# Performance work log

Measured on AMD Instinct MI355X. Metric: run time of the kernel, lower is better.

## Reference

```python
import jax, jax.numpy as jnp
import numpy as np

B, A, L, D, H = 8, 16, 80, 128, 6  # scenes, agents/scene, lanes/scene, feat dim, heads
LN_EPS = 1e-5


def _build_edges():
    hi_l, wi_l = [], []
    n_agt = B * A
    for b in range(B):
        ids = np.concatenate([np.arange(b * A, (b + 1) * A),
                              n_agt + np.arange(b * L, (b + 1) * L)])
        n = len(ids)
        hi_l.append(np.repeat(ids, n))  # 'd -> (d n)'
        wi_l.append(np.tile(ids, n))    # 'd -> (n d)'
    return (jnp.asarray(np.concatenate(hi_l), dtype=jnp.int32),
            jnp.asarray(np.concatenate(wi_l), dtype=jnp.int32))


def setup_inputs() -> dict:
    key = jax.random.key(0)
    ks = jax.random.split(key, 10)
    w = 0.05  # small init so exp(att) is well-behaved
    hi, wi = _build_edges()
    return {
        "agents": jax.random.normal(ks[0], (B * A, D), jnp.float32),
        "lanes": jax.random.normal(ks[1], (B * L, D), jnp.float32),
        "Wq": w * jax.random.normal(ks[2], (D, H * D), jnp.float32),
        "Wk": w * jax.random.normal(ks[3], (D, H * D), jnp.float32),
        "Wv": w * jax.random.normal(ks[4], (D, H * D), jnp.float32),
        "Wout1": w * jax.random.normal(ks[5], (H * D, D), jnp.float32),
        "Wout2": w * jax.random.normal(ks[6], (D, D), jnp.float32),
        "W1": w * jax.random.normal(ks[7], (D, D), jnp.float32),
        "ln_g": jnp.ones((D,), jnp.float32),
        "ln_b": jnp.zeros((D,), jnp.float32),
        "W2": w * jax.random.normal(ks[8], (D, D), jnp.float32),
        "hi": hi,
        "wi": wi,
    }


def _layernorm(x, g, b):
    mu = x.mean(-1, keepdims=True)
    var = ((x - mu) ** 2).mean(-1, keepdims=True)
    return (x - mu) * jax.lax.rsqrt(var + LN_EPS) * g + b


def reference(agents, lanes, Wq, Wk, Wv, Wout1, Wout2, W1, ln_g, ln_b, W2, hi, wi):
    nodes = jnp.concatenate([agents, lanes], axis=0)  # [N, D]
    N = nodes.shape[0]
    n_agt = agents.shape[0]
    scale = D ** -0.5

    src = nodes[hi]  # [E, D] (query side)
    dst = nodes[wi]  # [E, D] (key/value side)
    q = (src @ Wq).reshape(-1, H, D)
    k = (dst @ Wk).reshape(-1, H, D)
    v = jax.nn.relu(dst @ Wv).reshape(-1, H, D)

    att = jnp.einsum('ehd,ehd->eh', q, k) * scale          # [E, H]
    att = jnp.exp(att - att.max())                          # global-max-shifted exp (as in source)
    denom = jax.ops.segment_sum(att, hi, num_segments=N)    # [N, H]
    att = att / denom[hi]
    out = jax.ops.segment_sum(att[..., None] * v, hi, num_segments=N)  # [N, H, D]
    out = out.reshape(N, H * D)

    out = jax.nn.relu(out @ Wout1) @ Wout2                  # to_out
    h = _layernorm(nodes @ W1 + out, ln_g, ln_b)
    h = jax.nn.relu(h)
    h = h @ W2
    h = jax.nn.relu(h + nodes)                              # residual to pre-attention nodes
    return h[:n_agt]
```

## Files before the change

kernel.cpp:

```cpp
#include <hip/hip_runtime.h>
#include <math.h>

#define LN_EPS 1e-5f


__global__ __launch_bounds__(256) void k_prep(
    const float* __restrict__ Wq, const float* __restrict__ Wk,
    const float* __restrict__ agents, const float* __restrict__ W1,
    float* __restrict__ M, float* __restrict__ base)
{
    __shared__ float As[128][68];
    __shared__ float Bs[128][68];

    const int tid = threadIdx.x;
    const int bid = blockIdx.x;

    float* dst;
    if (bid < 24) {
        const int h = bid >> 2, quad = bid & 3;
        const int i0 = (quad >> 1) * 64, j0 = (quad & 1) * 64;
        const int c4 = tid & 15, kr = tid >> 4;
        #pragma unroll
        for (int ii = 0; ii < 8; ++ii) {
            const int k = kr + 16 * ii;
            *(float4*)&As[k][c4 * 4] =
                *(const float4*)(Wq + (size_t)k * 768 + h * 128 + i0 + c4 * 4);
            *(float4*)&Bs[k][c4 * 4] =
                *(const float4*)(Wk + (size_t)k * 768 + h * 128 + j0 + c4 * 4);
        }
        dst = M + (size_t)h * 16384 + (size_t)i0 * 128 + j0;
    } else {
        const int quad = bid - 24;
        const int i0 = (quad >> 1) * 64, j0 = (quad & 1) * 64;
        const int row = tid >> 2, kq = tid & 3;
        #pragma unroll
        for (int j = 0; j < 8; ++j) {
            const int k0 = kq * 4 + j * 16;
            const float4 a = *(const float4*)(agents + (size_t)(i0 + row) * 128 + k0);
            As[k0 + 0][row] = a.x; As[k0 + 1][row] = a.y;
            As[k0 + 2][row] = a.z; As[k0 + 3][row] = a.w;
        }
        const int c4 = tid & 15, kr = tid >> 4;
        #pragma unroll
        for (int ii = 0; ii < 8; ++ii) {
            const int k = kr + 16 * ii;
            *(float4*)&Bs[k][c4 * 4] =
                *(const float4*)(W1 + (size_t)k * 128 + j0 + c4 * 4);
        }
        dst = base + (size_t)i0 * 128 + j0;
    }
    __syncthreads();

    const int tx = tid & 15, ty = tid >> 4;
    float acc[4][4] = {};
    #pragma unroll 8
    for (int k = 0; k < 128; ++k) {
        const float4 a = *(const float4*)&As[k][ty * 4];
        const float4 b = *(const float4*)&Bs[k][tx * 4];
        const float av[4] = {a.x, a.y, a.z, a.w};
        #pragma unroll
        for (int i = 0; i < 4; ++i) {
            acc[i][0] += av[i] * b.x; acc[i][1] += av[i] * b.y;
            acc[i][2] += av[i] * b.z; acc[i][3] += av[i] * b.w;
        }
    }
    #pragma unroll
    for (int i = 0; i < 4; ++i)
        *(float4*)(dst + (size_t)(ty * 4 + i) * 128 + tx * 4) =
            make_float4(acc[i][0], acc[i][1], acc[i][2], acc[i][3]);
}

__global__ __launch_bounds__(512) void k_attn_f(
    const float* __restrict__ agents, const float* __restrict__ lanes,
    const float* __restrict__ Wv, const float* __restrict__ M,
    float* __restrict__ AO)
{
    __shared__ float Ns[96][132];
    __shared__ float Vh[96][68];
    __shared__ float Tt[16][132];
    __shared__ float Sm[16][100];

    const int tid = threadIdx.x;
    const int b = blockIdx.x;
    const int s = b / 12, r12 = b % 12;
    const int h = r12 >> 1, half = r12 & 1;

    for (int idx = tid; idx < 96 * 32; idx += 512) {
        const int n = idx >> 5, c4 = idx & 31;
        const float* src = (n < 16) ? (agents + (size_t)(s * 16 + n) * 128)
                                    : (lanes + (size_t)(s * 80 + n - 16) * 128);
        *(float4*)&Ns[n][c4 * 4] = *(const float4*)(src + c4 * 4);
    }
    __syncthreads();

    {
        const int c4 = tid & 15, rg = tid >> 4;
        const float* wp = Wv + h * 128 + half * 64 + c4 * 4;
        float4 a0 = make_float4(0,0,0,0), a1 = a0, a2 = a0;
        #pragma unroll 8
        for (int k = 0; k < 128; ++k) {
            const float4 w = *(const float4*)(wp + (size_t)k * 768);
            const float n0 = Ns[rg][k], n1 = Ns[rg + 32][k], n2 = Ns[rg + 64][k];
            a0.x += n0 * w.x; a0.y += n0 * w.y; a0.z += n0 * w.z; a0.w += n0 * w.w;
            a1.x += n1 * w.x; a1.y += n1 * w.y; a1.z += n1 * w.z; a1.w += n1 * w.w;
            a2.x += n2 * w.x; a2.y += n2 * w.y; a2.z += n2 * w.z; a2.w += n2 * w.w;
        }
        a0.x = fmaxf(a0.x, 0.f); a0.y = fmaxf(a0.y, 0.f);
        a0.z = fmaxf(a0.z, 0.f); a0.w = fmaxf(a0.w, 0.f);
        a1.x = fmaxf(a1.x, 0.f); a1.y = fmaxf(a1.y, 0.f);
        a1.z = fmaxf(a1.z, 0.f); a1.w = fmaxf(a1.w, 0.f);
        a2.x = fmaxf(a2.x, 0.f); a2.y = fmaxf(a2.y, 0.f);
        a2.z = fmaxf(a2.z, 0.f); a2.w = fmaxf(a2.w, 0.f);
        *(float4*)&Vh[rg][c4 * 4]      = a0;
        *(float4*)&Vh[rg + 32][c4 * 4] = a1;
        *(float4*)&Vh[rg + 64][c4 * 4] = a2;
    }

    {
        const int c4 = tid & 31, r = tid >> 5;
        const float* mp = M + (size_t)h * 16384 + c4 * 4;
        float4 acc = make_float4(0,0,0,0);
        #pragma unroll 8
        for (int k = 0; k < 128; ++k) {
            const float4 m4 = *(const float4*)(mp + (size_t)k * 128);
            const float a = Ns[r][k];
            acc.x += a * m4.x; acc.y += a * m4.y;
            acc.z += a * m4.z; acc.w += a * m4.w;
        }
        *(float4*)&Tt[r][c4 * 4] = acc;
    }
    __syncthreads();

    {
        const int i = tid >> 5, jc = tid & 31;
        float s0 = 0, s1 = 0, s2 = 0;
        #pragma unroll 4
        for (int kk = 0; kk < 32; ++kk) {
            const float4 t4 = *(const float4*)&Tt[i][kk * 4];
            const float4 a  = *(const float4*)&Ns[jc][kk * 4];
            const float4 bb = *(const float4*)&Ns[jc + 32][kk * 4];
            const float4 c  = *(const float4*)&Ns[jc + 64][kk * 4];
            s0 += t4.x*a.x  + t4.y*a.y  + t4.z*a.z  + t4.w*a.w;
            s1 += t4.x*bb.x + t4.y*bb.y + t4.z*bb.z + t4.w*bb.w;
            s2 += t4.x*c.x  + t4.y*c.y  + t4.z*c.z  + t4.w*c.w;
        }
        const float scale = 0.088388347648318447f;
        s0 *= scale; s1 *= scale; s2 *= scale;
        float m = fmaxf(fmaxf(s0, s1), s2);
        #pragma unroll
        for (int o = 16; o >= 1; o >>= 1) m = fmaxf(m, __shfl_xor(m, o, 32));
        const float e0 = __expf(s0 - m), e1 = __expf(s1 - m), e2 = __expf(s2 - m);
        float sum = e0 + e1 + e2;
        #pragma unroll
        for (int o = 16; o >= 1; o >>= 1) sum += __shfl_xor(sum, o, 32);
        const float inv = 1.0f / sum;
        Sm[i][jc]      = e0 * inv;
        Sm[i][jc + 32] = e1 * inv;
        Sm[i][jc + 64] = e2 * inv;
    }

    {
        const int i = tid >> 5, d2 = tid & 31;
        float o0 = 0, o1 = 0;
        #pragma unroll 4
        for (int j = 0; j < 96; ++j) {
            const float p = Sm[i][j];
            const float2 v = *(const float2*)&Vh[j][2 * d2];
            o0 += p * v.x; o1 += p * v.y;
        }
        float* dst = AO + (size_t)(s * 16 + i) * 768 + h * 128 + half * 64 + 2 * d2;
        *(float2*)dst = make_float2(o0, o1);
    }
}

__global__ __launch_bounds__(256) void k_f1(
    const float* __restrict__ AO, const float* __restrict__ Wout1,
    float* __restrict__ y1p)
{
    __shared__ float As[128][68];
    __shared__ float Bs[128][68];

    const int tid = threadIdx.x;
    const int b = blockIdx.x;
    const int s6 = b >> 2, quad = b & 3;
    const int m0 = (quad >> 1) * 64, n0 = (quad & 1) * 64;

    {
        const int row = tid >> 2, kq = tid & 3;
        #pragma unroll
        for (int j = 0; j < 8; ++j) {
            const int k0 = kq * 4 + j * 16;
            const float4 a =
                *(const float4*)(AO + (size_t)(m0 + row) * 768 + s6 * 128 + k0);
            As[k0 + 0][row] = a.x; As[k0 + 1][row] = a.y;
            As[k0 + 2][row] = a.z; As[k0 + 3][row] = a.w;
        }
    }
    {
        const int c4 = tid & 15, kr = tid >> 4;
        #pragma unroll
        for (int ii = 0; ii < 8; ++ii) {
            const int k = kr + 16 * ii;
            *(float4*)&Bs[k][c4 * 4] =
                *(const float4*)(Wout1 + (size_t)(s6 * 128 + k) * 128 + n0 + c4 * 4);
        }
    }
    __syncthreads();

    const int tx = tid & 15, ty = tid >> 4;
    float acc[4][4] = {};
    #pragma unroll 8
    for (int k = 0; k < 128; ++k) {
        const float4 a = *(const float4*)&As[k][ty * 4];
        const float4 bv = *(const float4*)&Bs[k][tx * 4];
        const float av[4] = {a.x, a.y, a.z, a.w};
        #pragma unroll
        for (int i = 0; i < 4; ++i) {
            acc[i][0] += av[i] * bv.x; acc[i][1] += av[i] * bv.y;
            acc[i][2] += av[i] * bv.z; acc[i][3] += av[i] * bv.w;
        }
    }
    float* dst = y1p + (size_t)s6 * 16384 + (size_t)m0 * 128 + n0;
    #pragma unroll
    for (int i = 0; i < 4; ++i)
        *(float4*)(dst + (size_t)(ty * 4 + i) * 128 + tx * 4) =
            make_float4(acc[i][0], acc[i][1], acc[i][2], acc[i][3]);
}

__global__ __launch_bounds__(512) void k_f2(
    const float* __restrict__ y1p, const float* __restrict__ base,
    const float* __restrict__ agents, const float* __restrict__ Wout2,
    const float* __restrict__ ln_g, const float* __restrict__ ln_b,
    const float* __restrict__ W2, float* __restrict__ out)
{
    const int a = blockIdx.x;
    const int tid = threadIdx.x;
    __shared__ float y1s[128];
    __shared__ float nr[128];
    __shared__ float br[128];
    __shared__ float hb[128];
    __shared__ float ps[512];
    __shared__ float red[4];

    if (tid < 32) {
        float4 acc = make_float4(0,0,0,0);
        #pragma unroll
        for (int s6 = 0; s6 < 6; ++s6) {
            const float4 v =
                *(const float4*)(y1p + (size_t)s6 * 16384 + (size_t)a * 128 + tid * 4);
            acc.x += v.x; acc.y += v.y; acc.z += v.z; acc.w += v.w;
        }
        y1s[tid * 4 + 0] = fmaxf(acc.x, 0.f); y1s[tid * 4 + 1] = fmaxf(acc.y, 0.f);
        y1s[tid * 4 + 2] = fmaxf(acc.z, 0.f); y1s[tid * 4 + 3] = fmaxf(acc.w, 0.f);
    } else if (tid < 64) {
        const int t = tid - 32;
        *(float4*)&nr[t * 4] = *(const float4*)(agents + (size_t)a * 128 + t * 4);
    } else if (tid < 96) {
        const int t = tid - 64;
        *(float4*)&br[t * 4] = *(const float4*)(base + (size_t)a * 128 + t * 4);
    }
    __syncthreads();

    const int d = tid & 127, g = tid >> 7;
    {
        const int k0 = g * 32;
        float p = 0.f;
        #pragma unroll 8
        for (int k = 0; k < 32; ++k)
            p += y1s[k0 + k] * Wout2[(size_t)(k0 + k) * 128 + d];
        ps[tid] = p;
    }
    __syncthreads();

    float tval = 0.f;
    if (tid < 128) tval = ps[d] + ps[128 + d] + ps[256 + d] + ps[384 + d] + br[d];
    float s1 = tval, s2 = tval * tval;
    #pragma unroll
    for (int o = 32; o >= 1; o >>= 1) { s1 += __shfl_xor(s1, o); s2 += __shfl_xor(s2, o); }
    if (tid < 128 && (tid & 63) == 0) {
        red[(tid >> 6) * 2] = s1; red[(tid >> 6) * 2 + 1] = s2;
    }
    __syncthreads();
    if (tid < 128) {
        const float S1 = red[0] + red[2], S2 = red[1] + red[3];
        const float mu  = S1 * (1.0f / 128.0f);
        const float var = S2 * (1.0f / 128.0f) - mu * mu;
        const float rin = rsqrtf(var + LN_EPS);
        hb[tid] = fmaxf((tval - mu) * rin * ln_g[tid] + ln_b[tid], 0.0f);
    }
    __syncthreads();

    {
        const int k0 = g * 32;
        float p = 0.f;
        #pragma unroll 8
        for (int k = 0; k < 32; ++k)
            p += hb[k0 + k] * W2[(size_t)(k0 + k) * 128 + d];
        ps[tid] = p;
    }
    __syncthreads();
    if (tid < 128)
        out[(size_t)a * 128 + d] =
            fmaxf(ps[d] + ps[128 + d] + ps[256 + d] + ps[384 + d] + nr[d], 0.0f);
}

extern "C" void kernel_launch(void* const* d_in, const int* in_sizes, int n_in,
                              void* d_out, int out_size, void* d_ws, size_t ws_size,
                              hipStream_t stream)
{
    const float* agents = (const float*)d_in[0];
    const float* lanes  = (const float*)d_in[1];
    const float* Wq     = (const float*)d_in[2];
    const float* Wk     = (const float*)d_in[3];
    const float* Wv     = (const float*)d_in[4];
    const float* Wout1  = (const float*)d_in[5];
    const float* Wout2  = (const float*)d_in[6];
    const float* W1     = (const float*)d_in[7];
    const float* ln_g   = (const float*)d_in[8];
    const float* ln_b   = (const float*)d_in[9];
    const float* W2     = (const float*)d_in[10];

    float* ws = (float*)d_ws;
    float* M    = ws;
    float* base = M + 6 * 16384;
    float* AO   = base + 16384;
    float* y1p  = AO + 128 * 768;
    float* outp = (float*)d_out;

    k_prep  <<<28, 256, 0, stream>>>(Wq, Wk, agents, W1, M, base);
    k_attn_f<<<96, 512, 0, stream>>>(agents, lanes, Wv, M, AO);
    k_f1    <<<24, 256, 0, stream>>>(AO, Wout1, y1p);
    k_f2    <<<128, 512, 0, stream>>>(y1p, base, agents, Wout2, ln_g, ln_b, W2, outp);
}
```

Baseline: 117.4 us.

## Precompute V and Q projections in a wide GEMM, compute Q·Wk^T in attention

The prep kernel no longer builds per-head Wq·Wk^T matrices. It now computes relu(nodes·Wv) for all nodes and agents·Wq with a 172-block tiled GEMM. The attention kernel loads the precomputed V and Q slices, and forms Q·Wk_h^T in 32-row chunks of Wk staged through shared memory, instead of running a per-block V projection and an M multiply. The Wout1 split-K GEMM is split more finely (48 blocks over 64-wide K slices), and the final kernel sums 12 partials instead of 6. This spreads the work over more blocks for parallelism, at the cost of writing V and Q through global memory and adding extra syncs in the attention kernel.

```diff
diff --git a/kernel.cpp b/kernel.cpp
--- a/kernel.cpp
+++ b/kernel.cpp
@@ -4,10 +4,11 @@
 #define LN_EPS 1e-5f
 
 
-__global__ __launch_bounds__(256) void k_prep(
-    const float* __restrict__ Wq, const float* __restrict__ Wk,
-    const float* __restrict__ agents, const float* __restrict__ W1,
-    float* __restrict__ M, float* __restrict__ base)
+__global__ __launch_bounds__(256) void k_qv(
+    const float* __restrict__ agents, const float* __restrict__ lanes,
+    const float* __restrict__ Wv, const float* __restrict__ Wq,
+    const float* __restrict__ W1, float* __restrict__ V,
+    float* __restrict__ Qb, float* __restrict__ base)
 {
     __shared__ float As[128][68];
     __shared__ float Bs[128][68];
@@ -15,39 +16,45 @@
     const int tid = threadIdx.x;
     const int bid = blockIdx.x;
 
-    float* dst;
-    if (bid < 24) {
-        const int h = bid >> 2, quad = bid & 3;
-        const int i0 = (quad >> 1) * 64, j0 = (quad & 1) * 64;
-        const int c4 = tid & 15, kr = tid >> 4;
-        #pragma unroll
-        for (int ii = 0; ii < 8; ++ii) {
-            const int k = kr + 16 * ii;
-            *(float4*)&As[k][c4 * 4] =
-                *(const float4*)(Wq + (size_t)k * 768 + h * 128 + i0 + c4 * 4);
-            *(float4*)&Bs[k][c4 * 4] =
-                *(const float4*)(Wk + (size_t)k * 768 + h * 128 + j0 + c4 * 4);
-        }
-        dst = M + (size_t)h * 16384 + (size_t)i0 * 128 + j0;
+    const float* W;
+    float* Out;
+    int r0, wc0, wstride, dstride;
+    bool dorelu = false;
+    if (bid < 144) {
+        const int br = bid % 12, bc = bid / 12;
+        r0 = br * 64; W = Wv; wc0 = bc * 64; wstride = 768;
+        Out = V; dstride = 768; dorelu = true;
+    } else if (bid < 168) {
+        const int idx = bid - 144;
+        r0 = (idx & 1) * 64; W = Wq; wc0 = (idx >> 1) * 64; wstride = 768;
+        Out = Qb; dstride = 768;
     } else {
-        const int quad = bid - 24;
-        const int i0 = (quad >> 1) * 64, j0 = (quad & 1) * 64;
-        const int row = tid >> 2, kq = tid & 3;
+        const int idx = bid - 168;
+        r0 = (idx & 1) * 64; W = W1; wc0 = (idx >> 1) * 64; wstride = 128;
+        Out = base; dstride = 128;
+    }
+
+    {
+        const int row = tid >> 2, kv = tid & 3;
+        const int gr = r0 + row;
+        const float* src = (gr < 128) ? (agents + (size_t)gr * 128)
+                                      : (lanes + (size_t)(gr - 128) * 128);
         #pragma unroll
         for (int j = 0; j < 8; ++j) {
-            const int k0 = kq * 4 + j * 16;
-            const float4 a = *(const float4*)(agents + (size_t)(i0 + row) * 128 + k0);
+            const int k0 = kv * 4 + j * 16;
+            const float4 a = *(const float4*)(src + k0);
             As[k0 + 0][row] = a.x; As[k0 + 1][row] = a.y;
             As[k0 + 2][row] = a.z; As[k0 + 3][row] = a.w;
         }
-        const int c4 = tid & 15, kr = tid >> 4;
-        #pragma unroll
-        for (int ii = 0; ii < 8; ++ii) {
-            const int k = kr + 16 * ii;
+    }
+    {
+        const int kr = tid >> 4, c4 = tid & 15;
+        #pragma unroll
+        for (int i = 0; i < 8; ++i) {
+            const int k = kr + 16 * i;
             *(float4*)&Bs[k][c4 * 4] =
-                *(const float4*)(W1 + (size_t)k * 128 + j0 + c4 * 4);
-        }
-        dst = base + (size_t)i0 * 128 + j0;
+                *(const float4*)(W + (size_t)k * wstride + wc0 + c4 * 4);
+        }
     }
     __syncthreads();
 
@@ -65,74 +72,85 @@
         }
     }
     #pragma unroll
-    for (int i = 0; i < 4; ++i)
-        *(float4*)(dst + (size_t)(ty * 4 + i) * 128 + tx * 4) =
-            make_float4(acc[i][0], acc[i][1], acc[i][2], acc[i][3]);
-}
-
-__global__ __launch_bounds__(512) void k_attn_f(
+    for (int i = 0; i < 4; ++i) {
+        float4 v = make_float4(acc[i][0], acc[i][1], acc[i][2], acc[i][3]);
+        if (dorelu) {
+            v.x = fmaxf(v.x, 0.f); v.y = fmaxf(v.y, 0.f);
+            v.z = fmaxf(v.z, 0.f); v.w = fmaxf(v.w, 0.f);
+        }
+        *(float4*)(Out + (size_t)(r0 + ty * 4 + i) * dstride + wc0 + tx * 4) = v;
+    }
+}
+
+__global__ __launch_bounds__(512) void k_attn2(
     const float* __restrict__ agents, const float* __restrict__ lanes,
-    const float* __restrict__ Wv, const float* __restrict__ M,
-    float* __restrict__ AO)
+    const float* __restrict__ Wk, const float* __restrict__ V,
+    const float* __restrict__ Qb, float* __restrict__ AO)
 {
     __shared__ float Ns[96][132];
     __shared__ float Vh[96][68];
+    __shared__ float Qs[16][132];
     __shared__ float Tt[16][132];
     __shared__ float Sm[16][100];
+    __shared__ float Wc[32][132];
 
     const int tid = threadIdx.x;
     const int b = blockIdx.x;
     const int s = b / 12, r12 = b % 12;
     const int h = r12 >> 1, half = r12 & 1;
 
-    for (int idx = tid; idx < 96 * 32; idx += 512) {
+    #pragma unroll
+    for (int ii = 0; ii < 6; ++ii) {
+        const int idx = tid + ii * 512;
         const int n = idx >> 5, c4 = idx & 31;
         const float* src = (n < 16) ? (agents + (size_t)(s * 16 + n) * 128)
                                     : (lanes + (size_t)(s * 80 + n - 16) * 128);
         *(float4*)&Ns[n][c4 * 4] = *(const float4*)(src + c4 * 4);
     }
-    __syncthreads();
-
-    {
-        const int c4 = tid & 15, rg = tid >> 4;
-        const float* wp = Wv + h * 128 + half * 64 + c4 * 4;
-        float4 a0 = make_float4(0,0,0,0), a1 = a0, a2 = a0;
-        #pragma unroll 8
-        for (int k = 0; k < 128; ++k) {
-            const float4 w = *(const float4*)(wp + (size_t)k * 768);
-            const float n0 = Ns[rg][k], n1 = Ns[rg + 32][k], n2 = Ns[rg + 64][k];
-            a0.x += n0 * w.x; a0.y += n0 * w.y; a0.z += n0 * w.z; a0.w += n0 * w.w;
-            a1.x += n1 * w.x; a1.y += n1 * w.y; a1.z += n1 * w.z; a1.w += n1 * w.w;
-            a2.x += n2 * w.x; a2.y += n2 * w.y; a2.z += n2 * w.z; a2.w += n2 * w.w;
-        }
-        a0.x = fmaxf(a0.x, 0.f); a0.y = fmaxf(a0.y, 0.f);
-        a0.z = fmaxf(a0.z, 0.f); a0.w = fmaxf(a0.w, 0.f);
-        a1.x = fmaxf(a1.x, 0.f); a1.y = fmaxf(a1.y, 0.f);
-        a1.z = fmaxf(a1.z, 0.f); a1.w = fmaxf(a1.w, 0.f);
-        a2.x = fmaxf(a2.x, 0.f); a2.y = fmaxf(a2.y, 0.f);
-        a2.z = fmaxf(a2.z, 0.f); a2.w = fmaxf(a2.w, 0.f);
-        *(float4*)&Vh[rg][c4 * 4]      = a0;
-        *(float4*)&Vh[rg + 32][c4 * 4] = a1;
-        *(float4*)&Vh[rg + 64][c4 * 4] = a2;
-    }
-
-    {
-        const int c4 = tid & 31, r = tid >> 5;
-        const float* mp = M + (size_t)h * 16384 + c4 * 4;
-        float4 acc = make_float4(0,0,0,0);
-        #pragma unroll 8
-        for (int k = 0; k < 128; ++k) {
-            const float4 m4 = *(const float4*)(mp + (size_t)k * 128);
-            const float a = Ns[r][k];
-            acc.x += a * m4.x; acc.y += a * m4.y;
-            acc.z += a * m4.z; acc.w += a * m4.w;
-        }
-        *(float4*)&Tt[r][c4 * 4] = acc;
-    }
-    __syncthreads();
-
-    {
-        const int i = tid >> 5, jc = tid & 31;
+    #pragma unroll
+    for (int ii = 0; ii < 3; ++ii) {
+        const int idx = tid + ii * 512;
+        const int n = idx >> 4, c4 = idx & 15;
+        const int g = (n < 16) ? (s * 16 + n) : (128 + s * 80 + (n - 16));
+        *(float4*)&Vh[n][c4 * 4] =
+            *(const float4*)(V + (size_t)g * 768 + h * 128 + half * 64 + c4 * 4);
+    }
+    {
+        const int r = tid >> 5, c4 = tid & 31;
+        *(float4*)&Qs[r][c4 * 4] =
+            *(const float4*)(Qb + (size_t)(s * 16 + r) * 768 + h * 128 + c4 * 4);
+    }
+    __syncthreads();
+
+    const int r = tid >> 5, kc = tid & 31;
+    for (int ck = 0; ck < 4; ++ck) {
+        {
+            const int i0 = tid * 2;
+            #pragma unroll
+            for (int ii = 0; ii < 2; ++ii) {
+                const int idx = i0 + ii;
+                const int row = idx >> 5, c4 = idx & 31;
+                *(float4*)&Wc[row][c4 * 4] =
+                    *(const float4*)(Wk + (size_t)(ck * 32 + row) * 768 +
+                                     h * 128 + c4 * 4);
+            }
+        }
+        __syncthreads();
+        {
+            float acc = 0.f;
+            #pragma unroll 8
+            for (int c4 = 0; c4 < 32; ++c4) {
+                const float4 q = *(const float4*)&Qs[r][c4 * 4];
+                const float4 w = *(const float4*)&Wc[kc][c4 * 4];
+                acc += q.x * w.x + q.y * w.y + q.z * w.z + q.w * w.w;
+            }
+            Tt[r][ck * 32 + kc] = acc;
+        }
+        __syncthreads();
+    }
+
+    {
+        const int i = r, jc = kc;
         float s0 = 0, s1 = 0, s2 = 0;
         #pragma unroll 4
         for (int kk = 0; kk < 32; ++kk) {
@@ -160,49 +178,49 @@
     }
 
     {
-        const int i = tid >> 5, d2 = tid & 31;
+        const int i = r, d = kc;
         float o0 = 0, o1 = 0;
         #pragma unroll 4
         for (int j = 0; j < 96; ++j) {
             const float p = Sm[i][j];
-            const float2 v = *(const float2*)&Vh[j][2 * d2];
+            const float2 v = *(const float2*)&Vh[j][2 * d];
             o0 += p * v.x; o1 += p * v.y;
         }
-        float* dst = AO + (size_t)(s * 16 + i) * 768 + h * 128 + half * 64 + 2 * d2;
+        float* dst = AO + (size_t)(s * 16 + i) * 768 + h * 128 + half * 64 + 2 * d;
         *(float2*)dst = make_float2(o0, o1);
     }
 }
 
-__global__ __launch_bounds__(256) void k_f1(
+__global__ __launch_bounds__(256) void k_f1w(
     const float* __restrict__ AO, const float* __restrict__ Wout1,
     float* __restrict__ y1p)
 {
-    __shared__ float As[128][68];
-    __shared__ float Bs[128][68];
+    __shared__ float As[64][68];
+    __shared__ float Bs[64][68];
 
     const int tid = threadIdx.x;
     const int b = blockIdx.x;
-    const int s6 = b >> 2, quad = b & 3;
+    const int ks = b >> 2, quad = b & 3;
     const int m0 = (quad >> 1) * 64, n0 = (quad & 1) * 64;
 
     {
         const int row = tid >> 2, kq = tid & 3;
         #pragma unroll
-        for (int j = 0; j < 8; ++j) {
+        for (int j = 0; j < 4; ++j) {
             const int k0 = kq * 4 + j * 16;
             const float4 a =
-                *(const float4*)(AO + (size_t)(m0 + row) * 768 + s6 * 128 + k0);
+                *(const float4*)(AO + (size_t)(m0 + row) * 768 + ks * 64 + k0);
             As[k0 + 0][row] = a.x; As[k0 + 1][row] = a.y;
             As[k0 + 2][row] = a.z; As[k0 + 3][row] = a.w;
         }
     }
     {
-        const int c4 = tid & 15, kr = tid >> 4;
-        #pragma unroll
-        for (int ii = 0; ii < 8; ++ii) {
-            const int k = kr + 16 * ii;
+        const int kr = tid >> 4, c4 = tid & 15;
+        #pragma unroll
+        for (int i = 0; i < 4; ++i) {
+            const int k = kr + 16 * i;
             *(float4*)&Bs[k][c4 * 4] =
-                *(const float4*)(Wout1 + (size_t)(s6 * 128 + k) * 128 + n0 + c4 * 4);
+                *(const float4*)(Wout1 + (size_t)(ks * 64 + k) * 128 + n0 + c4 * 4);
         }
     }
     __syncthreads();
@@ -210,7 +228,7 @@
     const int tx = tid & 15, ty = tid >> 4;
     float acc[4][4] = {};
     #pragma unroll 8
-    for (int k = 0; k < 128; ++k) {
+    for (int k = 0; k < 64; ++k) {
         const float4 a = *(const float4*)&As[k][ty * 4];
         const float4 bv = *(const float4*)&Bs[k][tx * 4];
         const float av[4] = {a.x, a.y, a.z, a.w};
@@ -220,7 +238,7 @@
             acc[i][2] += av[i] * bv.z; acc[i][3] += av[i] * bv.w;
         }
     }
-    float* dst = y1p + (size_t)s6 * 16384 + (size_t)m0 * 128 + n0;
+    float* dst = y1p + (size_t)ks * 16384 + (size_t)m0 * 128 + n0;
     #pragma unroll
     for (int i = 0; i < 4; ++i)
         *(float4*)(dst + (size_t)(ty * 4 + i) * 128 + tx * 4) =
@@ -245,9 +263,9 @@
     if (tid < 32) {
         float4 acc = make_float4(0,0,0,0);
         #pragma unroll
-        for (int s6 = 0; s6 < 6; ++s6) {
+        for (int ks = 0; ks < 12; ++ks) {
             const float4 v =
-                *(const float4*)(y1p + (size_t)s6 * 16384 + (size_t)a * 128 + tid * 4);
+                *(const float4*)(y1p + (size_t)ks * 16384 + (size_t)a * 128 + tid * 4);
             acc.x += v.x; acc.y += v.y; acc.z += v.z; acc.w += v.w;
         }
         y1s[tid * 4 + 0] = fmaxf(acc.x, 0.f); y1s[tid * 4 + 1] = fmaxf(acc.y, 0.f);
@@ -321,14 +339,15 @@
     const float* W2     = (const float*)d_in[10];
 
     float* ws = (float*)d_ws;
-    float* M    = ws;
-    float* base = M + 6 * 16384;
+    float* V    = ws;
+    float* Qb   = V + 768 * 768;
+    float* base = Qb + 128 * 768;
     float* AO   = base + 16384;
     float* y1p  = AO + 128 * 768;
     float* outp = (float*)d_out;
 
-    k_prep  <<<28, 256, 0, stream>>>(Wq, Wk, agents, W1, M, base);
-    k_attn_f<<<96, 512, 0, stream>>>(agents, lanes, Wv, M, AO);
-    k_f1    <<<24, 256, 0, stream>>>(AO, Wout1, y1p);
-    k_f2    <<<128, 512, 0, stream>>>(y1p, base, agents, Wout2, ln_g, ln_b, W2, outp);
-}
+    k_qv   <<<172, 256, 0, stream>>>(agents, lanes, Wv, Wq, W1, V, Qb, base);
+    k_attn2<<<96, 512, 0, stream>>>(agents, lanes, Wk, V, Qb, AO);
+    k_f1w  <<<48, 256, 0, stream>>>(AO, Wout1, y1p);
+    k_f2   <<<128, 512, 0, stream>>>(y1p, base, agents, Wout2, ln_g, ln_b, W2, outp);
+}
```

After: 107.9 us. 1.09x faster.

## Fuse pipeline into two kernels, computing Q/K projections inside attention

Applied to the files above, without the earlier changes.

Removes the precomputed Wq·Wk^T product kernel. The attention kernel now computes the query projection per agent, then the query-times-Wk^T product, staging weight chunks in shared memory. The Wout1 GEMM and the nodes·W1 term move into the per-agent tail kernel, so the partial-sum workspace buffers and two launches go away. This cuts launch count and intermediate global traffic, but each tail block now reads all of Wout1 and attention blocks redo some projection work.

```diff
diff --git a/kernel.cpp b/kernel.cpp
--- a/kernel.cpp
+++ b/kernel.cpp
@@ -4,135 +4,116 @@
 #define LN_EPS 1e-5f
 
 
-__global__ __launch_bounds__(256) void k_prep(
+__global__ __launch_bounds__(512) void k_attn_all(
+    const float* __restrict__ agents, const float* __restrict__ lanes,
     const float* __restrict__ Wq, const float* __restrict__ Wk,
-    const float* __restrict__ agents, const float* __restrict__ W1,
-    float* __restrict__ M, float* __restrict__ base)
-{
-    __shared__ float As[128][68];
-    __shared__ float Bs[128][68];
-
-    const int tid = threadIdx.x;
-    const int bid = blockIdx.x;
-
-    float* dst;
-    if (bid < 24) {
-        const int h = bid >> 2, quad = bid & 3;
-        const int i0 = (quad >> 1) * 64, j0 = (quad & 1) * 64;
-        const int c4 = tid & 15, kr = tid >> 4;
-        #pragma unroll
-        for (int ii = 0; ii < 8; ++ii) {
-            const int k = kr + 16 * ii;
-            *(float4*)&As[k][c4 * 4] =
-                *(const float4*)(Wq + (size_t)k * 768 + h * 128 + i0 + c4 * 4);
-            *(float4*)&Bs[k][c4 * 4] =
-                *(const float4*)(Wk + (size_t)k * 768 + h * 128 + j0 + c4 * 4);
-        }
-        dst = M + (size_t)h * 16384 + (size_t)i0 * 128 + j0;
-    } else {
-        const int quad = bid - 24;
-        const int i0 = (quad >> 1) * 64, j0 = (quad & 1) * 64;
-        const int row = tid >> 2, kq = tid & 3;
-        #pragma unroll
-        for (int j = 0; j < 8; ++j) {
-            const int k0 = kq * 4 + j * 16;
-            const float4 a = *(const float4*)(agents + (size_t)(i0 + row) * 128 + k0);
-            As[k0 + 0][row] = a.x; As[k0 + 1][row] = a.y;
-            As[k0 + 2][row] = a.z; As[k0 + 3][row] = a.w;
-        }
-        const int c4 = tid & 15, kr = tid >> 4;
-        #pragma unroll
-        for (int ii = 0; ii < 8; ++ii) {
-            const int k = kr + 16 * ii;
-            *(float4*)&Bs[k][c4 * 4] =
-                *(const float4*)(W1 + (size_t)k * 128 + j0 + c4 * 4);
-        }
-        dst = base + (size_t)i0 * 128 + j0;
-    }
-    __syncthreads();
-
-    const int tx = tid & 15, ty = tid >> 4;
-    float acc[4][4] = {};
-    #pragma unroll 8
-    for (int k = 0; k < 128; ++k) {
-        const float4 a = *(const float4*)&As[k][ty * 4];
-        const float4 b = *(const float4*)&Bs[k][tx * 4];
-        const float av[4] = {a.x, a.y, a.z, a.w};
-        #pragma unroll
-        for (int i = 0; i < 4; ++i) {
-            acc[i][0] += av[i] * b.x; acc[i][1] += av[i] * b.y;
-            acc[i][2] += av[i] * b.z; acc[i][3] += av[i] * b.w;
-        }
-    }
-    #pragma unroll
-    for (int i = 0; i < 4; ++i)
-        *(float4*)(dst + (size_t)(ty * 4 + i) * 128 + tx * 4) =
-            make_float4(acc[i][0], acc[i][1], acc[i][2], acc[i][3]);
-}
-
-__global__ __launch_bounds__(512) void k_attn_f(
-    const float* __restrict__ agents, const float* __restrict__ lanes,
-    const float* __restrict__ Wv, const float* __restrict__ M,
-    float* __restrict__ AO)
+    const float* __restrict__ Wv, float* __restrict__ AO)
 {
     __shared__ float Ns[96][132];
     __shared__ float Vh[96][68];
+    __shared__ float Qs[16][132];
     __shared__ float Tt[16][132];
     __shared__ float Sm[16][100];
+    __shared__ float Wc[64][132];
 
     const int tid = threadIdx.x;
     const int b = blockIdx.x;
     const int s = b / 12, r12 = b % 12;
     const int h = r12 >> 1, half = r12 & 1;
 
-    for (int idx = tid; idx < 96 * 32; idx += 512) {
+    #pragma unroll
+    for (int ii = 0; ii < 6; ++ii) {
+        const int idx = tid + ii * 512;
         const int n = idx >> 5, c4 = idx & 31;
         const float* src = (n < 16) ? (agents + (size_t)(s * 16 + n) * 128)
                                     : (lanes + (size_t)(s * 80 + n - 16) * 128);
         *(float4*)&Ns[n][c4 * 4] = *(const float4*)(src + c4 * 4);
     }
-    __syncthreads();
-
-    {
-        const int c4 = tid & 15, rg = tid >> 4;
-        const float* wp = Wv + h * 128 + half * 64 + c4 * 4;
-        float4 a0 = make_float4(0,0,0,0), a1 = a0, a2 = a0;
-        #pragma unroll 8
-        for (int k = 0; k < 128; ++k) {
-            const float4 w = *(const float4*)(wp + (size_t)k * 768);
-            const float n0 = Ns[rg][k], n1 = Ns[rg + 32][k], n2 = Ns[rg + 64][k];
-            a0.x += n0 * w.x; a0.y += n0 * w.y; a0.z += n0 * w.z; a0.w += n0 * w.w;
-            a1.x += n1 * w.x; a1.y += n1 * w.y; a1.z += n1 * w.z; a1.w += n1 * w.w;
-            a2.x += n2 * w.x; a2.y += n2 * w.y; a2.z += n2 * w.z; a2.w += n2 * w.w;
-        }
-        a0.x = fmaxf(a0.x, 0.f); a0.y = fmaxf(a0.y, 0.f);
-        a0.z = fmaxf(a0.z, 0.f); a0.w = fmaxf(a0.w, 0.f);
-        a1.x = fmaxf(a1.x, 0.f); a1.y = fmaxf(a1.y, 0.f);
-        a1.z = fmaxf(a1.z, 0.f); a1.w = fmaxf(a1.w, 0.f);
-        a2.x = fmaxf(a2.x, 0.f); a2.y = fmaxf(a2.y, 0.f);
-        a2.z = fmaxf(a2.z, 0.f); a2.w = fmaxf(a2.w, 0.f);
-        *(float4*)&Vh[rg][c4 * 4]      = a0;
-        *(float4*)&Vh[rg + 32][c4 * 4] = a1;
-        *(float4*)&Vh[rg + 64][c4 * 4] = a2;
-    }
-
-    {
-        const int c4 = tid & 31, r = tid >> 5;
-        const float* mp = M + (size_t)h * 16384 + c4 * 4;
-        float4 acc = make_float4(0,0,0,0);
-        #pragma unroll 8
-        for (int k = 0; k < 128; ++k) {
-            const float4 m4 = *(const float4*)(mp + (size_t)k * 128);
-            const float a = Ns[r][k];
-            acc.x += a * m4.x; acc.y += a * m4.y;
-            acc.z += a * m4.z; acc.w += a * m4.w;
-        }
-        *(float4*)&Tt[r][c4 * 4] = acc;
-    }
-    __syncthreads();
-
-    {
-        const int i = tid >> 5, jc = tid & 31;
+
+    const int r = tid >> 5, jc = tid & 31;
+
+    float q0 = 0, q1 = 0, q2 = 0, q3 = 0;
+    for (int ck = 0; ck < 2; ++ck) {
+        __syncthreads();
+        #pragma unroll
+        for (int ii = 0; ii < 4; ++ii) {
+            const int idx = tid + ii * 512;
+            const int row = idx >> 5, c4 = idx & 31;
+            *(float4*)&Wc[row][c4 * 4] =
+                *(const float4*)(Wq + (size_t)(ck * 64 + row) * 768 + h * 128 + c4 * 4);
+        }
+        __syncthreads();
+        #pragma unroll 4
+        for (int kk = 0; kk < 64; ++kk) {
+            const float a = Ns[r][ck * 64 + kk];
+            q0 += a * Wc[kk][jc];
+            q1 += a * Wc[kk][jc + 32];
+            q2 += a * Wc[kk][jc + 64];
+            q3 += a * Wc[kk][jc + 96];
+        }
+    }
+    Qs[r][jc] = q0; Qs[r][jc + 32] = q1; Qs[r][jc + 64] = q2; Qs[r][jc + 96] = q3;
+
+    const int rg = tid >> 4, cv = tid & 15;
+    float4 va0 = make_float4(0,0,0,0), va1 = va0, va2 = va0;
+    for (int ck = 0; ck < 2; ++ck) {
+        __syncthreads();
+        #pragma unroll
+        for (int ii = 0; ii < 2; ++ii) {
+            const int idx = tid + ii * 512;
+            const int row = idx >> 4, cc = idx & 15;
+            *(float4*)&Wc[row][cc * 4] =
+                *(const float4*)(Wv + (size_t)(ck * 64 + row) * 768 +
+                                 h * 128 + half * 64 + cc * 4);
+        }
+        __syncthreads();
+        #pragma unroll 4
+        for (int kk = 0; kk < 64; ++kk) {
+            const float4 w = *(const float4*)&Wc[kk][cv * 4];
+            const float n0 = Ns[rg][ck * 64 + kk];
+            const float n1 = Ns[rg + 32][ck * 64 + kk];
+            const float n2 = Ns[rg + 64][ck * 64 + kk];
+            va0.x += n0 * w.x; va0.y += n0 * w.y; va0.z += n0 * w.z; va0.w += n0 * w.w;
+            va1.x += n1 * w.x; va1.y += n1 * w.y; va1.z += n1 * w.z; va1.w += n1 * w.w;
+            va2.x += n2 * w.x; va2.y += n2 * w.y; va2.z += n2 * w.z; va2.w += n2 * w.w;
+        }
+    }
+    va0.x = fmaxf(va0.x, 0.f); va0.y = fmaxf(va0.y, 0.f);
+    va0.z = fmaxf(va0.z, 0.f); va0.w = fmaxf(va0.w, 0.f);
+    va1.x = fmaxf(va1.x, 0.f); va1.y = fmaxf(va1.y, 0.f);
+    va1.z = fmaxf(va1.z, 0.f); va1.w = fmaxf(va1.w, 0.f);
+    va2.x = fmaxf(va2.x, 0.f); va2.y = fmaxf(va2.y, 0.f);
+    va2.z = fmaxf(va2.z, 0.f); va2.w = fmaxf(va2.w, 0.f);
+    *(float4*)&Vh[rg][cv * 4]      = va0;
+    *(float4*)&Vh[rg + 32][cv * 4] = va1;
+    *(float4*)&Vh[rg + 64][cv * 4] = va2;
+
+    for (int ck = 0; ck < 2; ++ck) {
+        __syncthreads();
+        #pragma unroll
+        for (int ii = 0; ii < 4; ++ii) {
+            const int idx = tid + ii * 512;
+            const int row = idx >> 5, c4 = idx & 31;
+            *(float4*)&Wc[row][c4 * 4] =
+                *(const float4*)(Wk + (size_t)(ck * 64 + row) * 768 + h * 128 + c4 * 4);
+        }
+        __syncthreads();
+        float a1 = 0, a2 = 0;
+        #pragma unroll 4
+        for (int c4i = 0; c4i < 32; ++c4i) {
+            const float4 q  = *(const float4*)&Qs[r][c4i * 4];
+            const float4 w1 = *(const float4*)&Wc[jc][c4i * 4];
+            const float4 w2 = *(const float4*)&Wc[jc + 32][c4i * 4];
+            a1 += q.x * w1.x + q.y * w1.y + q.z * w1.z + q.w * w1.w;
+            a2 += q.x * w2.x + q.y * w2.y + q.z * w2.z + q.w * w2.w;
+        }
+        Tt[r][ck * 64 + jc]      = a1;
+        Tt[r][ck * 64 + 32 + jc] = a2;
+    }
+    __syncthreads();
+
+    {
+        const int i = r;
         float s0 = 0, s1 = 0, s2 = 0;
         #pragma unroll 4
         for (int kk = 0; kk < 32; ++kk) {
@@ -160,120 +141,71 @@
     }
 
     {
-        const int i = tid >> 5, d2 = tid & 31;
+        const int i = r, d = jc;
         float o0 = 0, o1 = 0;
         #pragma unroll 4
         for (int j = 0; j < 96; ++j) {
             const float p = Sm[i][j];
-            const float2 v = *(const float2*)&Vh[j][2 * d2];
+            const float2 v = *(const float2*)&Vh[j][2 * d];
             o0 += p * v.x; o1 += p * v.y;
         }
-        float* dst = AO + (size_t)(s * 16 + i) * 768 + h * 128 + half * 64 + 2 * d2;
+        float* dst = AO + (size_t)(s * 16 + i) * 768 + h * 128 + half * 64 + 2 * d;
         *(float2*)dst = make_float2(o0, o1);
     }
 }
 
-__global__ __launch_bounds__(256) void k_f1(
-    const float* __restrict__ AO, const float* __restrict__ Wout1,
-    float* __restrict__ y1p)
-{
-    __shared__ float As[128][68];
-    __shared__ float Bs[128][68];
-
-    const int tid = threadIdx.x;
-    const int b = blockIdx.x;
-    const int s6 = b >> 2, quad = b & 3;
-    const int m0 = (quad >> 1) * 64, n0 = (quad & 1) * 64;
-
-    {
-        const int row = tid >> 2, kq = tid & 3;
-        #pragma unroll
-        for (int j = 0; j < 8; ++j) {
-            const int k0 = kq * 4 + j * 16;
-            const float4 a =
-                *(const float4*)(AO + (size_t)(m0 + row) * 768 + s6 * 128 + k0);
-            As[k0 + 0][row] = a.x; As[k0 + 1][row] = a.y;
-            As[k0 + 2][row] = a.z; As[k0 + 3][row] = a.w;
-        }
-    }
-    {
-        const int c4 = tid & 15, kr = tid >> 4;
-        #pragma unroll
-        for (int ii = 0; ii < 8; ++ii) {
-            const int k = kr + 16 * ii;
-            *(float4*)&Bs[k][c4 * 4] =
-                *(const float4*)(Wout1 + (size_t)(s6 * 128 + k) * 128 + n0 + c4 * 4);
-        }
-    }
-    __syncthreads();
-
-    const int tx = tid & 15, ty = tid >> 4;
-    float acc[4][4] = {};
-    #pragma unroll 8
-    for (int k = 0; k < 128; ++k) {
-        const float4 a = *(const float4*)&As[k][ty * 4];
-        const float4 bv = *(const float4*)&Bs[k][tx * 4];
-        const float av[4] = {a.x, a.y, a.z, a.w};
-        #pragma unroll
-        for (int i = 0; i < 4; ++i) {
-            acc[i][0] += av[i] * bv.x; acc[i][1] += av[i] * bv.y;
-            acc[i][2] += av[i] * bv.z; acc[i][3] += av[i] * bv.w;
-        }
-    }
-    float* dst = y1p + (size_t)s6 * 16384 + (size_t)m0 * 128 + n0;
-    #pragma unroll
-    for (int i = 0; i < 4; ++i)
-        *(float4*)(dst + (size_t)(ty * 4 + i) * 128 + tx * 4) =
-            make_float4(acc[i][0], acc[i][1], acc[i][2], acc[i][3]);
-}
-
-__global__ __launch_bounds__(512) void k_f2(
-    const float* __restrict__ y1p, const float* __restrict__ base,
-    const float* __restrict__ agents, const float* __restrict__ Wout2,
-    const float* __restrict__ ln_g, const float* __restrict__ ln_b,
-    const float* __restrict__ W2, float* __restrict__ out)
+__global__ __launch_bounds__(512) void k_tail(
+    const float* __restrict__ AO, const float* __restrict__ agents,
+    const float* __restrict__ Wout1, const float* __restrict__ Wout2,
+    const float* __restrict__ W1, const float* __restrict__ ln_g,
+    const float* __restrict__ ln_b, const float* __restrict__ W2,
+    float* __restrict__ out)
 {
     const int a = blockIdx.x;
     const int tid = threadIdx.x;
+    __shared__ float AOs[768];
+    __shared__ float nr[128];
     __shared__ float y1s[128];
-    __shared__ float nr[128];
-    __shared__ float br[128];
     __shared__ float hb[128];
     __shared__ float ps[512];
     __shared__ float red[4];
 
-    if (tid < 32) {
-        float4 acc = make_float4(0,0,0,0);
-        #pragma unroll
-        for (int s6 = 0; s6 < 6; ++s6) {
-            const float4 v =
-                *(const float4*)(y1p + (size_t)s6 * 16384 + (size_t)a * 128 + tid * 4);
-            acc.x += v.x; acc.y += v.y; acc.z += v.z; acc.w += v.w;
-        }
-        y1s[tid * 4 + 0] = fmaxf(acc.x, 0.f); y1s[tid * 4 + 1] = fmaxf(acc.y, 0.f);
-        y1s[tid * 4 + 2] = fmaxf(acc.z, 0.f); y1s[tid * 4 + 3] = fmaxf(acc.w, 0.f);
-    } else if (tid < 64) {
-        const int t = tid - 32;
+    if (tid < 192) {
+        *(float4*)&AOs[tid * 4] = *(const float4*)(AO + (size_t)a * 768 + tid * 4);
+    } else if (tid < 224) {
+        const int t = tid - 192;
         *(float4*)&nr[t * 4] = *(const float4*)(agents + (size_t)a * 128 + t * 4);
-    } else if (tid < 96) {
-        const int t = tid - 64;
-        *(float4*)&br[t * 4] = *(const float4*)(base + (size_t)a * 128 + t * 4);
     }
     __syncthreads();
 
     const int d = tid & 127, g = tid >> 7;
-    {
-        const int k0 = g * 32;
+
+    {
+        const int k0 = g * 192;
         float p = 0.f;
         #pragma unroll 8
-        for (int k = 0; k < 32; ++k)
-            p += y1s[k0 + k] * Wout2[(size_t)(k0 + k) * 128 + d];
+        for (int k = 0; k < 192; ++k)
+            p += AOs[k0 + k] * Wout1[(size_t)(k0 + k) * 128 + d];
         ps[tid] = p;
     }
     __syncthreads();
+    if (tid < 128) y1s[d] = fmaxf(ps[d] + ps[128 + d] + ps[256 + d] + ps[384 + d], 0.f);
+    __syncthreads();
+
+    {
+        const float* src = (g < 2) ? y1s : nr;
+        const float* Wm  = (g < 2) ? Wout2 : W1;
+        const int k0 = (g & 1) * 64;
+        float p = 0.f;
+        #pragma unroll 8
+        for (int k = 0; k < 64; ++k)
+            p += src[k0 + k] * Wm[(size_t)(k0 + k) * 128 + d];
+        ps[tid] = p;
+    }
+    __syncthreads();
 
     float tval = 0.f;
-    if (tid < 128) tval = ps[d] + ps[128 + d] + ps[256 + d] + ps[384 + d] + br[d];
+    if (tid < 128) tval = ps[d] + ps[128 + d] + ps[256 + d] + ps[384 + d];
     float s1 = tval, s2 = tval * tval;
     #pragma unroll
     for (int o = 32; o >= 1; o >>= 1) { s1 += __shfl_xor(s1, o); s2 += __shfl_xor(s2, o); }
@@ -286,7 +218,7 @@
         const float mu  = S1 * (1.0f / 128.0f);
         const float var = S2 * (1.0f / 128.0f) - mu * mu;
         const float rin = rsqrtf(var + LN_EPS);
-        hb[tid] = fmaxf((tval - mu) * rin * ln_g[tid] + ln_b[tid], 0.0f);
+        hb[d] = fmaxf((tval - mu) * rin * ln_g[d] + ln_b[d], 0.0f);
     }
     __syncthreads();
 
@@ -320,15 +252,10 @@
     const float* ln_b   = (const float*)d_in[9];
     const float* W2     = (const float*)d_in[10];
 
-    float* ws = (float*)d_ws;
-    float* M    = ws;
-    float* base = M + 6 * 16384;
-    float* AO   = base + 16384;
-    float* y1p  = AO + 128 * 768;
+    float* AO   = (float*)d_ws;
     float* outp = (float*)d_out;
 
-    k_prep  <<<28, 256, 0, stream>>>(Wq, Wk, agents, W1, M, base);
-    k_attn_f<<<96, 512, 0, stream>>>(agents, lanes, Wv, M, AO);
-    k_f1    <<<24, 256, 0, stream>>>(AO, Wout1, y1p);
-    k_f2    <<<128, 512, 0, stream>>>(y1p, base, agents, Wout2, ln_g, ln_b, W2, outp);
+    k_attn_all<<<96, 512, 0, stream>>>(agents, lanes, Wq, Wk, Wv, AO);
+    k_tail    <<<128, 512, 0, stream>>>(AO, agents, Wout1, Wout2, W1,
+                                        ln_g, ln_b, W2, outp);
 }
```

Measured after the change: 112.7 us. 1.04x faster.
